# Optimization experiments

Measured on AMD Instinct MI355X. Metric: run time of the kernel, lower is better.

The kernel has to match this reference:

```python
import jax, jax.numpy as jnp
import numpy as np

LEAKY_ALPHA = 0.2  # TF default for tf.nn.leaky_relu

def setup_inputs() -> dict:
    key = jax.random.key(0)
    k1, k2, k3 = jax.random.split(key, 3)
    B, N, D = 8192, 2048, 128
    patient_features = jax.random.normal(k1, (B, D), dtype=jnp.float32)
    disease_nodes = jax.random.normal(k2, (N, D), dtype=jnp.float32)
    attn_kernel = jax.random.normal(k3, (2 * D, 1), dtype=jnp.float32)
    return {"patient_features": patient_features,
            "disease_nodes": disease_nodes,
            "attn_kernel": attn_kernel}

def reference(patient_features, disease_nodes, attn_kernel):
    # patient_features: [B, D]; disease_nodes: [N, D]; attn_kernel: [2D, 1]
    D = patient_features.shape[-1]
    a_p = attn_kernel[:D, 0]   # [D] acts on the patient half of the concat
    a_n = attn_kernel[D:, 0]   # [D] acts on the disease-node half
    # concat([p, n]) @ a  ==  p @ a_p  +  n @ a_n  (exact decomposition)
    scores = (patient_features @ a_p)[:, None] + (disease_nodes @ a_n)[None, :]  # [B, N]
    attn_weights = jax.nn.softmax(jax.nn.leaky_relu(scores, LEAKY_ALPHA), axis=1)  # [B, N]
    node_influence = attn_weights @ disease_nodes  # [B, D]
    return patient_features + node_influence
```

## Files before the change

kernel.cpp:

```cpp
#include <hip/hip_runtime.h>
#include <hip/hip_bf16.h>

#define LEAKY 0.2f
#define B_TOT 8192
#define N_TOT 2048
#define D_TOT 128
#define BM 16

typedef float f32x4 __attribute__((ext_vector_type(4)));
typedef short bf16x8 __attribute__((ext_vector_type(8)));
typedef unsigned short u16x8 __attribute__((ext_vector_type(8)));

static __device__ __forceinline__ unsigned short f2bf(float x) {
    return __builtin_bit_cast(unsigned short, __float2bfloat16(x));
}

__global__ __launch_bounds__(256) void prep_kernel(const float* __restrict__ disease,
                                                   const float* __restrict__ ak,
                                                   float* __restrict__ q,
                                                   uint4* __restrict__ DnTf) {
    __shared__ float tile[32][129];
    __shared__ float a_s[D_TOT];
    const int tid = threadIdx.x;
    const int b = blockIdx.x;
    const int r0 = b * 32;

    if (tid < D_TOT) a_s[tid] = ak[D_TOT + tid];
    #pragma unroll
    for (int t = 0; t < 4; ++t) {
        int idx = tid + t * 256;
        int row = idx >> 5;
        int cv = (idx & 31) * 4;
        float4 v = *(const float4*)(disease + (size_t)(r0 + row) * D_TOT + cv);
        tile[row][cv] = v.x; tile[row][cv + 1] = v.y;
        tile[row][cv + 2] = v.z; tile[row][cv + 3] = v.w;
    }
    __syncthreads();

    const int wave = tid >> 6, lane = tid & 63;
    #pragma unroll
    for (int rr = 0; rr < 8; ++rr) {
        int r = wave * 8 + rr;
        float s = tile[r][lane] * a_s[lane] + tile[r][lane + 64] * a_s[lane + 64];
        #pragma unroll
        for (int off = 32; off; off >>= 1) s += __shfl_xor(s, off);
        if (lane == 0) q[r0 + r] = s;
    }

    #pragma unroll
    for (int h = 0; h < 2; ++h) {
        const int c  = tid + h * 256;
        const int kg = c >> 7;
        const int col = c & 127;
        const int ct = col >> 4, cl = col & 15;
        unsigned u[4];
        #pragma unroll
        for (int jj = 0; jj < 4; ++jj) {
            unsigned lo = f2bf(tile[kg * 8 + 2 * jj][col]);
            unsigned hi = f2bf(tile[kg * 8 + 2 * jj + 1][col]);
            u[jj] = lo | (hi << 16);
        }
        DnTf[((size_t)b * 8 + ct) * 64 + kg * 16 + cl] = make_uint4(u[0], u[1], u[2], u[3]);
    }
}

__global__ __launch_bounds__(1024, 8) void gat_mfma(const float* __restrict__ patient,
                                                    const float* __restrict__ ak,
                                                    const float* __restrict__ q,
                                                    const uint4* __restrict__ DnTf,
                                                    float* __restrict__ out) {
    __shared__ __align__(16) float eq1_s[N_TOT];
    __shared__ __align__(16) float eq2_s[N_TOT];
    __shared__ float red_s[7][2][1024];
    __shared__ float a_s[D_TOT];
    __shared__ float p_s[BM], E1_s[BM], E2_s[BM], S_s[BM];
    __shared__ float red16[16];

    const int tid  = threadIdx.x;
    const int wave = tid >> 6;
    const int lane = tid & 63;
    const int b0   = blockIdx.x * BM;

    if (tid < D_TOT) a_s[tid] = ak[tid];
    __syncthreads();

    float mx = -1e30f;
    for (int i = tid; i < N_TOT; i += 1024) {
        float qq = q[i];
        eq1_s[i] = __expf(qq);
        eq2_s[i] = __expf(LEAKY * qq);
        mx = fmaxf(mx, qq);
    }
    #pragma unroll
    for (int off = 32; off; off >>= 1) mx = fmaxf(mx, __shfl_xor(mx, off));
    if (lane == 0) red16[wave] = mx;

    {
        const float* pr = patient + (size_t)(b0 + wave) * D_TOT;
        float s = pr[lane] * a_s[lane] + pr[lane + 64] * a_s[lane + 64];
        #pragma unroll
        for (int off = 32; off; off >>= 1) s += __shfl_xor(s, off);
        if (lane == 0) p_s[wave] = s;
    }
    __syncthreads();

    if (tid < BM) {
        float qmax = red16[0];
        #pragma unroll
        for (int i = 1; i < 16; ++i) qmax = fmaxf(qmax, red16[i]);
        const float pv = p_s[tid];
        const float xm = pv + qmax;
        const float m = fmaxf(xm, LEAKY * xm);
        E1_s[tid] = __expf(pv - m);
        E2_s[tid] = __expf(LEAKY * pv - m);
    }
    __syncthreads();

    {
        const float E1 = E1_s[wave], E2 = E2_s[wave];
        float s = 0.f;
        for (int n = lane; n < N_TOT; n += 64)
            s += fmaxf(E1 * eq1_s[n], E2 * eq2_s[n]);
        #pragma unroll
        for (int off = 32; off; off >>= 1) s += __shfl_xor(s, off);
        if (lane == 0) S_s[wave] = s;
    }
    __syncthreads();

    const int cl = lane & 15;
    const int kg = lane >> 4;
    const int cw = wave & 1;
    const int kq = wave >> 1;

    const float E1A = E1_s[cl], E2A = E2_s[cl];
    const uint4* fbase = DnTf + (size_t)(cw * 4) * 64 + lane;

    f32x4 acc[4] = {};

    for (int kt = kq * 8; kt < kq * 8 + 8; ++kt) {
        const uint4* fp = fbase + (size_t)kt * 512;
        const uint4 b0v = fp[0];
        const uint4 b1v = fp[64];
        const uint4 b2v = fp[128];
        const uint4 b3v = fp[192];

        const int gk = kt * 32 + kg * 8;
        u16x8 aw;
        {
            const float4 e1 = *(const float4*)&eq1_s[gk];
            const float4 e2 = *(const float4*)&eq2_s[gk];
            aw[0] = f2bf(fmaxf(E1A * e1.x, E2A * e2.x));
            aw[1] = f2bf(fmaxf(E1A * e1.y, E2A * e2.y));
            aw[2] = f2bf(fmaxf(E1A * e1.z, E2A * e2.z));
            aw[3] = f2bf(fmaxf(E1A * e1.w, E2A * e2.w));
        }
        {
            const float4 e1 = *(const float4*)&eq1_s[gk + 4];
            const float4 e2 = *(const float4*)&eq2_s[gk + 4];
            aw[4] = f2bf(fmaxf(E1A * e1.x, E2A * e2.x));
            aw[5] = f2bf(fmaxf(E1A * e1.y, E2A * e2.y));
            aw[6] = f2bf(fmaxf(E1A * e1.z, E2A * e2.z));
            aw[7] = f2bf(fmaxf(E1A * e1.w, E2A * e2.w));
        }
        const bf16x8 a0 = __builtin_bit_cast(bf16x8, aw);

        acc[0] = __builtin_amdgcn_mfma_f32_16x16x32_bf16(a0, __builtin_bit_cast(bf16x8, b0v), acc[0], 0, 0, 0);
        acc[1] = __builtin_amdgcn_mfma_f32_16x16x32_bf16(a0, __builtin_bit_cast(bf16x8, b1v), acc[1], 0, 0, 0);
        acc[2] = __builtin_amdgcn_mfma_f32_16x16x32_bf16(a0, __builtin_bit_cast(bf16x8, b2v), acc[2], 0, 0, 0);
        acc[3] = __builtin_amdgcn_mfma_f32_16x16x32_bf16(a0, __builtin_bit_cast(bf16x8, b3v), acc[3], 0, 0, 0);
    }

    __syncthreads();
    if (kq > 0) {
        float* rb = &red_s[kq - 1][cw][0];
        #pragma unroll
        for (int t = 0; t < 4; ++t)
            #pragma unroll
            for (int i = 0; i < 4; ++i)
                rb[t * 256 + (kg * 4 + i) * 16 + cl] = acc[t][i];
    }
    __syncthreads();
    if (kq == 0) {
        #pragma unroll
        for (int t = 0; t < 4; ++t)
            #pragma unroll
            for (int i = 0; i < 4; ++i) {
                const int idx = t * 256 + (kg * 4 + i) * 16 + cl;
                float s = acc[t][i];
                #pragma unroll
                for (int j = 0; j < 7; ++j) s += red_s[j][cw][idx];
                acc[t][i] = s;
            }
        float inv[4];
        #pragma unroll
        for (int i = 0; i < 4; ++i) inv[i] = 1.0f / S_s[kg * 4 + i];
        #pragma unroll
        for (int t = 0; t < 4; ++t)
            #pragma unroll
            for (int i = 0; i < 4; ++i) {
                const int row = b0 + kg * 4 + i;
                const int col = cw * 64 + t * 16 + cl;
                out[(size_t)row * D_TOT + col] =
                    patient[(size_t)row * D_TOT + col] + acc[t][i] * inv[i];
            }
    }
}

__global__ __launch_bounds__(256) void pq_fb(const float* __restrict__ patient,
                                             const float* __restrict__ disease,
                                             const float* __restrict__ ak,
                                             float* __restrict__ p,
                                             float* __restrict__ q) {
    int gid  = blockIdx.x * blockDim.x + threadIdx.x;
    int wid  = gid >> 6;
    int lane = gid & 63;
    const float* src;
    const float* a;
    float* dst;
    if (wid < B_TOT) {
        src = patient + (size_t)wid * D_TOT; a = ak; dst = p + wid;
    } else {
        src = disease + (size_t)(wid - B_TOT) * D_TOT; a = ak + D_TOT; dst = q + (wid - B_TOT);
    }
    float s = src[lane] * a[lane] + src[lane + 64] * a[lane + 64];
    #pragma unroll
    for (int off = 32; off; off >>= 1) s += __shfl_xor(s, off);
    if (lane == 0) *dst = s;
}

#define FBP 16
#define FNT 256
__global__ __launch_bounds__(256) void gat_fb(const float* __restrict__ patient,
                                              const float* __restrict__ disease,
                                              const float* __restrict__ p,
                                              const float* __restrict__ q,
                                              float* __restrict__ out) {
    __shared__ float q_s[N_TOT];
    __shared__ float w_s[FBP][FNT];
    __shared__ float m_s[FBP], S_s[FBP], pp_s[FBP];
    const int tid = threadIdx.x;
    const int b0  = blockIdx.x * FBP;
    for (int i = tid; i < N_TOT; i += 256) q_s[i] = q[i];
    if (tid < FBP) pp_s[tid] = p[b0 + tid];
    __syncthreads();
    const int wave = tid >> 6, lane = tid & 63;
    for (int pi = wave * 4; pi < wave * 4 + 4; ++pi) {
        float pp = pp_s[pi];
        float mx = -1e30f;
        for (int n = lane; n < N_TOT; n += 64) {
            float x = pp + q_s[n]; x = x > 0.0f ? x : LEAKY * x; mx = fmaxf(mx, x);
        }
        #pragma unroll
        for (int off = 32; off; off >>= 1) mx = fmaxf(mx, __shfl_xor(mx, off));
        float sum = 0.0f;
        for (int n = lane; n < N_TOT; n += 64) {
            float x = pp + q_s[n]; x = x > 0.0f ? x : LEAKY * x; sum += __expf(x - mx);
        }
        #pragma unroll
        for (int off = 32; off; off >>= 1) sum += __shfl_xor(sum, off);
        if (lane == 0) { m_s[pi] = mx; S_s[pi] = sum; }
    }
    __syncthreads();
    const int d2 = tid & 31;
    const int pg = tid >> 5;
    const int p0 = 2 * pg, p1 = 2 * pg + 1;
    float4 acc0 = make_float4(0.f, 0.f, 0.f, 0.f);
    float4 acc1 = make_float4(0.f, 0.f, 0.f, 0.f);
    for (int n0 = 0; n0 < N_TOT; n0 += FNT) {
        __syncthreads();
        for (int i = tid; i < FBP * FNT; i += 256) {
            int pi = i >> 8;
            int nt = i & (FNT - 1);
            float x = pp_s[pi] + q_s[n0 + nt];
            x = x > 0.0f ? x : LEAKY * x;
            w_s[pi][nt] = __expf(x - m_s[pi]);
        }
        __syncthreads();
        const float* drow = disease + (size_t)n0 * D_TOT + d2 * 4;
        #pragma unroll 4
        for (int nt = 0; nt < FNT; ++nt) {
            float4 dv = *reinterpret_cast<const float4*>(drow + (size_t)nt * D_TOT);
            float w0 = w_s[p0][nt];
            float w1 = w_s[p1][nt];
            acc0.x += w0 * dv.x; acc0.y += w0 * dv.y; acc0.z += w0 * dv.z; acc0.w += w0 * dv.w;
            acc1.x += w1 * dv.x; acc1.y += w1 * dv.y; acc1.z += w1 * dv.z; acc1.w += w1 * dv.w;
        }
    }
    const float inv0 = 1.0f / S_s[p0];
    const float inv1 = 1.0f / S_s[p1];
    {
        size_t off = (size_t)(b0 + p0) * D_TOT + d2 * 4;
        float4 pf = *reinterpret_cast<const float4*>(patient + off);
        float4 o;
        o.x = pf.x + acc0.x * inv0; o.y = pf.y + acc0.y * inv0;
        o.z = pf.z + acc0.z * inv0; o.w = pf.w + acc0.w * inv0;
        *reinterpret_cast<float4*>(reinterpret_cast<float*>(out) + off) = o;
    }
    {
        size_t off = (size_t)(b0 + p1) * D_TOT + d2 * 4;
        float4 pf = *reinterpret_cast<const float4*>(patient + off);
        float4 o;
        o.x = pf.x + acc1.x * inv1; o.y = pf.y + acc1.y * inv1;
        o.z = pf.z + acc1.z * inv1; o.w = pf.w + acc1.w * inv1;
        *reinterpret_cast<float4*>(reinterpret_cast<float*>(out) + off) = o;
    }
}

extern "C" void kernel_launch(void* const* d_in, const int* in_sizes, int n_in,
                              void* d_out, int out_size, void* d_ws, size_t ws_size,
                              hipStream_t stream) {
    const float* patient = (const float*)d_in[0];
    const float* disease = (const float*)d_in[1];
    const float* ak      = (const float*)d_in[2];
    float* out = (float*)d_out;

    const size_t need_fast = (size_t)512 * 1024 + 8192;
    if (ws_size >= need_fast) {
        uint4* DnTf = (uint4*)d_ws;
        float* q    = (float*)((char*)d_ws + 512 * 1024);
        prep_kernel<<<N_TOT / 32, 256, 0, stream>>>(disease, ak, q, DnTf);
        gat_mfma<<<B_TOT / BM, 1024, 0, stream>>>(patient, ak, q, DnTf, out);
    } else {
        float* p = (float*)d_ws;
        float* q = p + B_TOT;
        pq_fb<<<(B_TOT + N_TOT) / 4, 256, 0, stream>>>(patient, disease, ak, p, q);
        gat_fb<<<B_TOT / FBP, 256, 0, stream>>>(patient, disease, p, q, out);
    }
}
```

Before: 26.68 us.

## Sort disease nodes by score and use prefix sums instead of a dense attention GEMM

Adds a kernel that computes the disease scores, ranks them with an O(N^2) counting sort and writes the disease rows in score order. Because leaky_relu of p+q only changes slope at q = -p, each patient's weighted sum splits into an exp(q)-weighted sum over nodes above a threshold plus an exp(0.2q)-weighted sum over nodes below it. A new fp32 streaming kernel builds these prefix and suffix sums once per block of 32 patients. Each patient then finds its split point by binary search, and snapshots taken at those points give exact per-patient partial sums. This replaces the per-patient bf16 MFMA product over all nodes, but each block still streams the full sorted fp32 disease matrix, and the unnormalised exponentials risk overflow for larger score ranges. The new path needs a larger workspace, and the older MFMA path is kept as a fallback.

```diff
diff --git a/kernel.cpp b/kernel.cpp
--- a/kernel.cpp
+++ b/kernel.cpp
@@ -13,6 +13,194 @@
 
 static __device__ __forceinline__ unsigned short f2bf(float x) {
     return __builtin_bit_cast(unsigned short, __float2bfloat16(x));
+}
+
+__global__ __launch_bounds__(512) void qrank_kernel(const float* __restrict__ disease,
+                                                    const float* __restrict__ ak,
+                                                    float* __restrict__ sortedq,
+                                                    float* __restrict__ Dsorted) {
+    __shared__ float q_s[N_TOT];
+    __shared__ float a_s[D_TOT];
+    __shared__ int   rank_l[32];
+    const int tid = threadIdx.x;
+    if (tid < D_TOT) a_s[tid] = ak[D_TOT + tid];
+    __syncthreads();
+
+    const int hw = tid >> 5, hl = tid & 31;
+    const float4 av = *(const float4*)(a_s + hl * 4);
+    for (int r = hw; r < N_TOT; r += 64) {
+        float s[4];
+        #pragma unroll
+        for (int u = 0; u < 4; ++u) {
+            const float4 v = *(const float4*)(disease + (size_t)(r + u * 16) * D_TOT + hl * 4);
+            s[u] = v.x * av.x + v.y * av.y + v.z * av.z + v.w * av.w;
+        }
+        #pragma unroll
+        for (int u = 0; u < 4; ++u) {
+            s[u] += __shfl_xor(s[u], 16); s[u] += __shfl_xor(s[u], 8);
+            s[u] += __shfl_xor(s[u], 4);  s[u] += __shfl_xor(s[u], 2);
+            s[u] += __shfl_xor(s[u], 1);
+        }
+        if (hl == 0) {
+            #pragma unroll
+            for (int u = 0; u < 4; ++u) q_s[r + u * 16] = s[u];
+        }
+    }
+    __syncthreads();
+
+    const int kl = tid >> 4, sub = tid & 15;
+    const int k = blockIdx.x * 32 + kl;
+    const float qk = q_s[k];
+    int cnt = 0;
+    const int j0 = sub * 128;
+    #pragma unroll 8
+    for (int j = j0; j < j0 + 128; ++j) {
+        const float qj = q_s[j];
+        cnt += (qj < qk || (qj == qk && j < k)) ? 1 : 0;
+    }
+    cnt += __shfl_xor(cnt, 1); cnt += __shfl_xor(cnt, 2);
+    cnt += __shfl_xor(cnt, 4); cnt += __shfl_xor(cnt, 8);
+    if (sub == 0) { sortedq[cnt] = qk; rank_l[kl] = cnt; }
+    __syncthreads();
+
+    const int rl = tid >> 4, tc = tid & 15;
+    const int dst = rank_l[rl];
+    const float* srcp = disease + (size_t)(blockIdx.x * 32 + rl) * D_TOT + tc * 8;
+    float* dstp = Dsorted + (size_t)dst * D_TOT + tc * 8;
+    const float4 v0 = *(const float4*)(srcp);
+    const float4 v1 = *(const float4*)(srcp + 4);
+    *(float4*)(dstp)     = v0;
+    *(float4*)(dstp + 4) = v1;
+}
+
+__global__ __launch_bounds__(1024) void gat_stream(const float* __restrict__ patient,
+                                                   const float* __restrict__ Dsorted,
+                                                   const float* __restrict__ ak,
+                                                   const float* __restrict__ sortedq,
+                                                   float* __restrict__ out) {
+    __shared__ float sq[N_TOT];
+    __shared__ float e1l[N_TOT], e2l[N_TOT];
+    __shared__ unsigned mask[N_TOT];
+    __shared__ __align__(16) float snap1[32][128], snap2[32][128];
+    __shared__ __align__(16) float sseg1[33][128], sseg2[33][128];
+    __shared__ float a_s[D_TOT];
+    __shared__ float p_s[32], E1_s[32], E2_s[32], inv_s[32];
+    __shared__ int   c_s[32];
+
+    const int tid  = threadIdx.x;
+    const int wave = tid >> 6;
+    const int lane = tid & 63;
+    const int b0   = blockIdx.x * 32;
+
+    for (int i = tid; i < N_TOT; i += 1024) {
+        const float s = sortedq[i];
+        sq[i]  = s;
+        e1l[i] = __expf(s);
+        e2l[i] = __expf(LEAKY * s);
+        mask[i] = 0u;
+    }
+    if (tid < D_TOT) a_s[tid] = ak[tid];
+    __syncthreads();
+
+    #pragma unroll
+    for (int rr = 0; rr < 2; ++rr) {
+        const int row = wave * 2 + rr;
+        const float* pr = patient + (size_t)(b0 + row) * D_TOT;
+        float s = pr[lane] * a_s[lane] + pr[lane + 64] * a_s[lane + 64];
+        #pragma unroll
+        for (int off = 32; off; off >>= 1) s += __shfl_xor(s, off);
+        if (lane == 0) p_s[row] = s;
+    }
+    __syncthreads();
+
+    #pragma unroll
+    for (int rr = 0; rr < 2; ++rr) {
+        const int row = wave * 2 + rr;
+        const float pv = p_s[row];
+        const float qmax = sq[N_TOT - 1];
+        const float xm = pv + qmax;
+        const float m = fmaxf(xm, LEAKY * xm);
+        const float E1 = __expf(pv - m);
+        const float E2 = __expf(LEAKY * pv - m);
+        float s = 0.f;
+        for (int n = lane; n < N_TOT; n += 64)
+            s += fmaxf(E1 * e1l[n], E2 * e2l[n]);
+        #pragma unroll
+        for (int off = 32; off; off >>= 1) s += __shfl_xor(s, off);
+        if (lane == 0) { E1_s[row] = E1; E2_s[row] = E2; inv_s[row] = 1.0f / s; }
+    }
+    if (tid < 32) {
+        const float thr = -p_s[tid];
+        int lo = 0, hi = N_TOT;
+        while (lo < hi) {
+            const int mid = (lo + hi) >> 1;
+            if (sq[mid] <= thr) lo = mid + 1; else hi = mid;
+        }
+        c_s[tid] = lo;
+        if (lo < N_TOT) atomicOr(&mask[lo], 1u << tid);
+    }
+    __syncthreads();
+
+    {
+        const int seg = tid >> 5;
+        const int c0  = (tid & 31) * 4;
+        const int jbase = seg * 64;
+        float4 r1 = make_float4(0.f, 0.f, 0.f, 0.f);
+        float4 r2 = make_float4(0.f, 0.f, 0.f, 0.f);
+        #pragma unroll 4
+        for (int jj = 63; jj >= 0; --jj) {
+            const int j = jbase + jj;
+            const float4 d = *(const float4*)(Dsorted + (size_t)j * D_TOT + c0);
+            const float e1 = e1l[j], e2 = e2l[j];
+            r1.x = fmaf(e1, d.x, r1.x); r1.y = fmaf(e1, d.y, r1.y);
+            r1.z = fmaf(e1, d.z, r1.z); r1.w = fmaf(e1, d.w, r1.w);
+            r2.x = fmaf(e2, d.x, r2.x); r2.y = fmaf(e2, d.y, r2.y);
+            r2.z = fmaf(e2, d.z, r2.z); r2.w = fmaf(e2, d.w, r2.w);
+            unsigned mk = mask[j];
+            while (mk) {
+                const int r = __ffs(mk) - 1;
+                mk &= mk - 1;
+                *(float4*)&snap1[r][c0] = r1;
+                *(float4*)&snap2[r][c0] = r2;
+            }
+        }
+        *(float4*)&sseg1[seg][c0] = r1;
+        *(float4*)&sseg2[seg][c0] = r2;
+    }
+    __syncthreads();
+
+    if (tid < 128) {
+        float a1 = 0.f, a2 = 0.f;
+        sseg1[32][tid] = 0.f; sseg2[32][tid] = 0.f;
+        #pragma unroll
+        for (int s = 31; s >= 0; --s) {
+            a1 += sseg1[s][tid]; sseg1[s][tid] = a1;
+            a2 += sseg2[s][tid]; sseg2[s][tid] = a2;
+        }
+    }
+    __syncthreads();
+
+    {
+        const int row = tid >> 5;
+        const int c0 = (tid & 31) * 4;
+        const int gr = b0 + row;
+        const int c = c_s[row];
+        const bool has = (c < N_TOT);
+        const int sg1 = has ? ((c >> 6) + 1) : 32;
+        const float E1 = E1_s[row], E2 = E2_s[row], inv = inv_s[row];
+        const float4 pat = *(const float4*)&patient[(size_t)gr * D_TOT + c0];
+        float o[4];
+        #pragma unroll
+        for (int i = 0; i < 4; ++i) {
+            const int col = c0 + i;
+            const float suf1 = (has ? snap1[row][col] : 0.f) + sseg1[sg1][col];
+            const float suf2 = (has ? snap2[row][col] : 0.f) + sseg2[sg1][col];
+            const float pre2 = sseg2[0][col] - suf2;
+            const float pi = (i == 0) ? pat.x : (i == 1) ? pat.y : (i == 2) ? pat.z : pat.w;
+            o[i] = pi + (E1 * suf1 + E2 * pre2) * inv;
+        }
+        *(float4*)&out[(size_t)gr * D_TOT + c0] = make_float4(o[0], o[1], o[2], o[3]);
+    }
 }
 
 __global__ __launch_bounds__(256) void prep_kernel(const float* __restrict__ disease,
@@ -24,7 +212,6 @@
     const int tid = threadIdx.x;
     const int b = blockIdx.x;
     const int r0 = b * 32;
-
     if (tid < D_TOT) a_s[tid] = ak[D_TOT + tid];
     #pragma unroll
     for (int t = 0; t < 4; ++t) {
@@ -36,7 +223,6 @@
         tile[row][cv + 2] = v.z; tile[row][cv + 3] = v.w;
     }
     __syncthreads();
-
     const int wave = tid >> 6, lane = tid & 63;
     #pragma unroll
     for (int rr = 0; rr < 8; ++rr) {
@@ -46,7 +232,6 @@
         for (int off = 32; off; off >>= 1) s += __shfl_xor(s, off);
         if (lane == 0) q[r0 + r] = s;
     }
-
     #pragma unroll
     for (int h = 0; h < 2; ++h) {
         const int c  = tid + h * 256;
@@ -75,15 +260,12 @@
     __shared__ float a_s[D_TOT];
     __shared__ float p_s[BM], E1_s[BM], E2_s[BM], S_s[BM];
     __shared__ float red16[16];
-
     const int tid  = threadIdx.x;
     const int wave = tid >> 6;
     const int lane = tid & 63;
     const int b0   = blockIdx.x * BM;
-
     if (tid < D_TOT) a_s[tid] = ak[tid];
     __syncthreads();
-
     float mx = -1e30f;
     for (int i = tid; i < N_TOT; i += 1024) {
         float qq = q[i];
@@ -94,7 +276,6 @@
     #pragma unroll
     for (int off = 32; off; off >>= 1) mx = fmaxf(mx, __shfl_xor(mx, off));
     if (lane == 0) red16[wave] = mx;
-
     {
         const float* pr = patient + (size_t)(b0 + wave) * D_TOT;
         float s = pr[lane] * a_s[lane] + pr[lane + 64] * a_s[lane + 64];
@@ -103,7 +284,6 @@
         if (lane == 0) p_s[wave] = s;
     }
     __syncthreads();
-
     if (tid < BM) {
         float qmax = red16[0];
         #pragma unroll
@@ -115,7 +295,6 @@
         E2_s[tid] = __expf(LEAKY * pv - m);
     }
     __syncthreads();
-
     {
         const float E1 = E1_s[wave], E2 = E2_s[wave];
         float s = 0.f;
@@ -126,24 +305,19 @@
         if (lane == 0) S_s[wave] = s;
     }
     __syncthreads();
-
     const int cl = lane & 15;
     const int kg = lane >> 4;
     const int cw = wave & 1;
     const int kq = wave >> 1;
-
     const float E1A = E1_s[cl], E2A = E2_s[cl];
     const uint4* fbase = DnTf + (size_t)(cw * 4) * 64 + lane;
-
     f32x4 acc[4] = {};
-
     for (int kt = kq * 8; kt < kq * 8 + 8; ++kt) {
         const uint4* fp = fbase + (size_t)kt * 512;
         const uint4 b0v = fp[0];
         const uint4 b1v = fp[64];
         const uint4 b2v = fp[128];
         const uint4 b3v = fp[192];
-
         const int gk = kt * 32 + kg * 8;
         u16x8 aw;
         {
@@ -163,13 +337,11 @@
             aw[7] = f2bf(fmaxf(E1A * e1.w, E2A * e2.w));
         }
         const bf16x8 a0 = __builtin_bit_cast(bf16x8, aw);
-
         acc[0] = __builtin_amdgcn_mfma_f32_16x16x32_bf16(a0, __builtin_bit_cast(bf16x8, b0v), acc[0], 0, 0, 0);
         acc[1] = __builtin_amdgcn_mfma_f32_16x16x32_bf16(a0, __builtin_bit_cast(bf16x8, b1v), acc[1], 0, 0, 0);
         acc[2] = __builtin_amdgcn_mfma_f32_16x16x32_bf16(a0, __builtin_bit_cast(bf16x8, b2v), acc[2], 0, 0, 0);
         acc[3] = __builtin_amdgcn_mfma_f32_16x16x32_bf16(a0, __builtin_bit_cast(bf16x8, b3v), acc[3], 0, 0, 0);
     }
-
     __syncthreads();
     if (kq > 0) {
         float* rb = &red_s[kq - 1][cw][0];
@@ -313,11 +485,19 @@
     const float* disease = (const float*)d_in[1];
     const float* ak      = (const float*)d_in[2];
     float* out = (float*)d_out;
-
-    const size_t need_fast = (size_t)512 * 1024 + 8192;
+    char* w = (char*)d_ws;
+
+    const size_t need_fast = 8192 + (size_t)N_TOT * D_TOT * 4;
+    const size_t need_mid  = (size_t)512 * 1024 + 8192;
+
     if (ws_size >= need_fast) {
+        float* sq = (float*)w;
+        float* Ds = (float*)(w + 8192);
+        qrank_kernel<<<N_TOT / 32, 512, 0, stream>>>(disease, ak, sq, Ds);
+        gat_stream<<<B_TOT / 32, 1024, 0, stream>>>(patient, Ds, ak, sq, out);
+    } else if (ws_size >= need_mid) {
         uint4* DnTf = (uint4*)d_ws;
-        float* q    = (float*)((char*)d_ws + 512 * 1024);
+        float* q    = (float*)(w + 512 * 1024);
         prep_kernel<<<N_TOT / 32, 256, 0, stream>>>(disease, ak, q, DnTf);
         gat_mfma<<<B_TOT / BM, 1024, 0, stream>>>(patient, ak, q, DnTf, out);
     } else {
```

After: 60.15 us. +125.5%, slower.

## Switch to 32x32x16 MFMA with 32-row patient tiles and repacked disease layout

Applied to the files above, without the earlier changes.

Doubles the patient rows per block from 16 to 32 and replaces the 16x16x32 bf16 MFMAs with 32x32x16 bf16 MFMAs. The prep kernel repacks the transposed bf16 disease fragments to match the new operand layout. The aim is to halve the number of blocks, so each block's per-block overhead (exp tables over all N, q max reduction) is amortised over twice as many rows and disease data is reused more. In exchange the reduction buffer in shared memory doubles to about 130 KB, and the launch bound drops to 4 blocks, which reduces occupancy.

```diff
diff --git a/kernel.cpp b/kernel.cpp
--- a/kernel.cpp
+++ b/kernel.cpp
@@ -5,9 +5,9 @@
 #define B_TOT 8192
 #define N_TOT 2048
 #define D_TOT 128
-#define BM 16
-
-typedef float f32x4 __attribute__((ext_vector_type(4)));
+#define BM 32
+
+typedef float f32x16 __attribute__((ext_vector_type(16)));
 typedef short bf16x8 __attribute__((ext_vector_type(8)));
 typedef unsigned short u16x8 __attribute__((ext_vector_type(8)));
 
@@ -49,29 +49,31 @@
 
     #pragma unroll
     for (int h = 0; h < 2; ++h) {
-        const int c  = tid + h * 256;
-        const int kg = c >> 7;
-        const int col = c & 127;
-        const int ct = col >> 4, cl = col & 15;
+        const int ci = tid + h * 256;
+        const int f  = ci >> 6;
+        const int ln = ci & 63;
+        const int lt = f >> 2, ct = f & 3;
+        const int g  = ln >> 5, c = ln & 31;
+        const int rb = lt * 16 + g * 8;
         unsigned u[4];
         #pragma unroll
         for (int jj = 0; jj < 4; ++jj) {
-            unsigned lo = f2bf(tile[kg * 8 + 2 * jj][col]);
-            unsigned hi = f2bf(tile[kg * 8 + 2 * jj + 1][col]);
+            unsigned lo = f2bf(tile[rb + 2 * jj][ct * 32 + c]);
+            unsigned hi = f2bf(tile[rb + 2 * jj + 1][ct * 32 + c]);
             u[jj] = lo | (hi << 16);
         }
-        DnTf[((size_t)b * 8 + ct) * 64 + kg * 16 + cl] = make_uint4(u[0], u[1], u[2], u[3]);
-    }
-}
-
-__global__ __launch_bounds__(1024, 8) void gat_mfma(const float* __restrict__ patient,
-                                                    const float* __restrict__ ak,
-                                                    const float* __restrict__ q,
-                                                    const uint4* __restrict__ DnTf,
-                                                    float* __restrict__ out) {
+        DnTf[((size_t)(2 * b + lt) * 4 + ct) * 64 + ln] = make_uint4(u[0], u[1], u[2], u[3]);
+    }
+}
+
+__global__ __launch_bounds__(1024, 4) void gat_mfma32(const float* __restrict__ patient,
+                                                      const float* __restrict__ ak,
+                                                      const float* __restrict__ q,
+                                                      const uint4* __restrict__ DnTf,
+                                                      float* __restrict__ out) {
     __shared__ __align__(16) float eq1_s[N_TOT];
     __shared__ __align__(16) float eq2_s[N_TOT];
-    __shared__ float red_s[7][2][1024];
+    __shared__ float red_s[7][2][2048];
     __shared__ float a_s[D_TOT];
     __shared__ float p_s[BM], E1_s[BM], E2_s[BM], S_s[BM];
     __shared__ float red16[16];
@@ -95,12 +97,14 @@
     for (int off = 32; off; off >>= 1) mx = fmaxf(mx, __shfl_xor(mx, off));
     if (lane == 0) red16[wave] = mx;
 
-    {
-        const float* pr = patient + (size_t)(b0 + wave) * D_TOT;
+    #pragma unroll
+    for (int rr = 0; rr < 2; ++rr) {
+        const int row = wave * 2 + rr;
+        const float* pr = patient + (size_t)(b0 + row) * D_TOT;
         float s = pr[lane] * a_s[lane] + pr[lane + 64] * a_s[lane + 64];
         #pragma unroll
         for (int off = 32; off; off >>= 1) s += __shfl_xor(s, off);
-        if (lane == 0) p_s[wave] = s;
+        if (lane == 0) p_s[row] = s;
     }
     __syncthreads();
 
@@ -116,35 +120,35 @@
     }
     __syncthreads();
 
-    {
-        const float E1 = E1_s[wave], E2 = E2_s[wave];
+    #pragma unroll
+    for (int rr = 0; rr < 2; ++rr) {
+        const int row = wave * 2 + rr;
+        const float E1 = E1_s[row], E2 = E2_s[row];
         float s = 0.f;
         for (int n = lane; n < N_TOT; n += 64)
             s += fmaxf(E1 * eq1_s[n], E2 * eq2_s[n]);
         #pragma unroll
         for (int off = 32; off; off >>= 1) s += __shfl_xor(s, off);
-        if (lane == 0) S_s[wave] = s;
-    }
-    __syncthreads();
-
-    const int cl = lane & 15;
-    const int kg = lane >> 4;
-    const int cw = wave & 1;
-    const int kq = wave >> 1;
-
-    const float E1A = E1_s[cl], E2A = E2_s[cl];
-    const uint4* fbase = DnTf + (size_t)(cw * 4) * 64 + lane;
-
-    f32x4 acc[4] = {};
-
-    for (int kt = kq * 8; kt < kq * 8 + 8; ++kt) {
-        const uint4* fp = fbase + (size_t)kt * 512;
-        const uint4 b0v = fp[0];
-        const uint4 b1v = fp[64];
-        const uint4 b2v = fp[128];
-        const uint4 b3v = fp[192];
-
-        const int gk = kt * 32 + kg * 8;
+        if (lane == 0) S_s[row] = s;
+    }
+    __syncthreads();
+
+    const int c31 = lane & 31;
+    const int g   = lane >> 5;
+    const int cw  = wave & 1;
+    const int kq  = wave >> 1;
+
+    const float E1A = E1_s[c31], E2A = E2_s[c31];
+    const uint4* fbase = DnTf + (size_t)(cw * 2) * 64 + lane;
+
+    f32x16 acc0{}, acc1{};
+
+    for (int kt = kq * 16; kt < kq * 16 + 16; ++kt) {
+        const uint4* fp = fbase + (size_t)kt * 256;
+        const uint4 bv0 = fp[0];
+        const uint4 bv1 = fp[64];
+
+        const int gk = kt * 16 + g * 8;
         u16x8 aw;
         {
             const float4 e1 = *(const float4*)&eq1_s[gk];
@@ -164,45 +168,38 @@
         }
         const bf16x8 a0 = __builtin_bit_cast(bf16x8, aw);
 
-        acc[0] = __builtin_amdgcn_mfma_f32_16x16x32_bf16(a0, __builtin_bit_cast(bf16x8, b0v), acc[0], 0, 0, 0);
-        acc[1] = __builtin_amdgcn_mfma_f32_16x16x32_bf16(a0, __builtin_bit_cast(bf16x8, b1v), acc[1], 0, 0, 0);
-        acc[2] = __builtin_amdgcn_mfma_f32_16x16x32_bf16(a0, __builtin_bit_cast(bf16x8, b2v), acc[2], 0, 0, 0);
-        acc[3] = __builtin_amdgcn_mfma_f32_16x16x32_bf16(a0, __builtin_bit_cast(bf16x8, b3v), acc[3], 0, 0, 0);
+        acc0 = __builtin_amdgcn_mfma_f32_32x32x16_bf16(a0, __builtin_bit_cast(bf16x8, bv0), acc0, 0, 0, 0);
+        acc1 = __builtin_amdgcn_mfma_f32_32x32x16_bf16(a0, __builtin_bit_cast(bf16x8, bv1), acc1, 0, 0, 0);
     }
 
     __syncthreads();
     if (kq > 0) {
         float* rb = &red_s[kq - 1][cw][0];
         #pragma unroll
-        for (int t = 0; t < 4; ++t)
+        for (int rg = 0; rg < 16; ++rg) {
+            const int rl = (rg & 3) + 8 * (rg >> 2) + 4 * g;
+            rb[rl * 64 + c31]      = acc0[rg];
+            rb[rl * 64 + 32 + c31] = acc1[rg];
+        }
+    }
+    __syncthreads();
+    if (kq == 0) {
+        #pragma unroll
+        for (int rg = 0; rg < 16; ++rg) {
+            const int rl = (rg & 3) + 8 * (rg >> 2) + 4 * g;
+            float s0 = acc0[rg], s1 = acc1[rg];
             #pragma unroll
-            for (int i = 0; i < 4; ++i)
-                rb[t * 256 + (kg * 4 + i) * 16 + cl] = acc[t][i];
-    }
-    __syncthreads();
-    if (kq == 0) {
-        #pragma unroll
-        for (int t = 0; t < 4; ++t)
-            #pragma unroll
-            for (int i = 0; i < 4; ++i) {
-                const int idx = t * 256 + (kg * 4 + i) * 16 + cl;
-                float s = acc[t][i];
-                #pragma unroll
-                for (int j = 0; j < 7; ++j) s += red_s[j][cw][idx];
-                acc[t][i] = s;
+            for (int j = 0; j < 7; ++j) {
+                s0 += red_s[j][cw][rl * 64 + c31];
+                s1 += red_s[j][cw][rl * 64 + 32 + c31];
             }
-        float inv[4];
-        #pragma unroll
-        for (int i = 0; i < 4; ++i) inv[i] = 1.0f / S_s[kg * 4 + i];
-        #pragma unroll
-        for (int t = 0; t < 4; ++t)
-            #pragma unroll
-            for (int i = 0; i < 4; ++i) {
-                const int row = b0 + kg * 4 + i;
-                const int col = cw * 64 + t * 16 + cl;
-                out[(size_t)row * D_TOT + col] =
-                    patient[(size_t)row * D_TOT + col] + acc[t][i] * inv[i];
-            }
+            const float inv = 1.0f / S_s[rl];
+            const int row = b0 + rl;
+            const int colA = cw * 64 + c31;
+            const int colB = colA + 32;
+            out[(size_t)row * D_TOT + colA] = patient[(size_t)row * D_TOT + colA] + s0 * inv;
+            out[(size_t)row * D_TOT + colB] = patient[(size_t)row * D_TOT + colB] + s1 * inv;
+        }
     }
 }
 
@@ -319,7 +316,7 @@
         uint4* DnTf = (uint4*)d_ws;
         float* q    = (float*)((char*)d_ws + 512 * 1024);
         prep_kernel<<<N_TOT / 32, 256, 0, stream>>>(disease, ak, q, DnTf);
-        gat_mfma<<<B_TOT / BM, 1024, 0, stream>>>(patient, ak, q, DnTf, out);
+        gat_mfma32<<<B_TOT / BM, 1024, 0, stream>>>(patient, ak, q, DnTf, out);
     } else {
         float* p = (float*)d_ws;
         float* q = p + B_TOT;
```

After: 26.05 us (median of 2 runs). 1.02x faster.
